# Kernel tuning notes

Measured on AMD Instinct MI355X. Metric: run time of the kernel, lower is better.

Reference implementation:

```python
import jax, jax.numpy as jnp
import numpy as np

N, F, H, K, O = 16384, 64, 128, 16, 10


def setup_inputs() -> dict:
    key = jax.random.key(0)
    ks = jax.random.split(key, 12)
    s = lambda fan: 1.0 / np.sqrt(fan)
    return {
        "x": jax.random.normal(ks[0], (N, F), dtype=jnp.float32),
        "edge_index": jax.random.randint(ks[1], (2, N * 8), 0, N),  # unused by forward
        "mlp_w1": jax.random.normal(ks[2], (2 * F, H), dtype=jnp.float32) * s(2 * F),
        "mlp_b1": jnp.zeros((H,), jnp.float32),
        "mlp_w2": jax.random.normal(ks[3], (H, H), dtype=jnp.float32) * s(H),
        "mlp_b2": jnp.zeros((H,), jnp.float32),
        "gcn_w": jax.random.normal(ks[4], (H, H), dtype=jnp.float32) * s(H),
        "gcn_b": jnp.zeros((H,), jnp.float32),
        "gnn_out_w": jax.random.normal(ks[5], (H, H), dtype=jnp.float32) * s(H),
        "gnn_out_b": jnp.zeros((H,), jnp.float32),
        "out_w": jax.random.normal(ks[6], (H, O), dtype=jnp.float32) * s(H),
        "out_b": jnp.zeros((O,), jnp.float32),
        "k": K,
    }


def _forward(x, mlp_w1, mlp_b1, mlp_w2, mlp_b2, gcn_w, gcn_b,
             gnn_out_w, gnn_out_b, out_w, out_b, k):
    n = x.shape[0]
    # ---- dynamic kNN graph in feature space (includes self, dist 0) ----
    sq = jnp.sum(x * x, axis=-1)                       # [N]
    d2 = sq[:, None] + sq[None, :] - 2.0 * (x @ x.T)   # [N,N] squared dists
    _, idx = jax.lax.top_k(-d2, k)                     # [N,k] neighbor (source) ids per query
    # ---- EdgeConv message: MLP(cat(x_i, x_j - x_i)), max-aggregate over k ----
    x_j = x[idx]                                       # [N,k,F]
    x_i = jnp.broadcast_to(x[:, None, :], x_j.shape)   # [N,k,F]
    m = jnp.concatenate([x_i, x_j - x_i], axis=-1)     # [N,k,2F]
    m = jax.nn.relu(m @ mlp_w1 + mlp_b1)
    m = jax.nn.log_softmax(m @ mlp_w2 + mlp_b2, axis=-1)
    h = jnp.max(m, axis=1)                             # [N,H] max aggregation
    # ---- GCNConv on the kNN edge_index (+ self loops, symmetric norm) ----
    loop = jnp.arange(n)
    src = jnp.concatenate([idx.reshape(-1), loop])     # sources (x_j)
    dst = jnp.concatenate([jnp.repeat(loop, k), loop]) # targets (x_i)
    deg = jax.ops.segment_sum(jnp.ones_like(src, h.dtype), dst, num_segments=n)
    dinv = jax.lax.rsqrt(jnp.maximum(deg, 1.0))
    norm = dinv[src] * dinv[dst]                       # [E]
    hw = h @ gcn_w                                     # [N,H]
    h = jax.ops.segment_sum(norm[:, None] * hw[src], dst, num_segments=n) + gcn_b
    # ---- inner GNN output head (Linear + Softmax) ----
    h = jax.nn.softmax(h @ gnn_out_w + gnn_out_b, axis=-1)
    # ---- GNN_Combo output head (Linear + Softmax) ----
    return jax.nn.softmax(h @ out_w + out_b, axis=-1)  # [N,O]


def reference(x, edge_index, mlp_w1, mlp_b1, mlp_w2, mlp_b2, gcn_w, gcn_b,
              gnn_out_w, gnn_out_b, out_w, out_b, k):
    # edge_index is accepted by GNN_Combo.forward but unused (kNN graph replaces it)
    del edge_index
    return _forward(x, mlp_w1, mlp_b1, mlp_w2, mlp_b2, gcn_w, gcn_b,
                    gnn_out_w, gnn_out_b, out_w, out_b, k)
```

## Files before the change

kernel.cpp:

```cpp
#include <hip/hip_runtime.h>
#include <hip/hip_fp16.h>
#include <cfloat>
#include <cmath>
#include <string.h>


#define N_NODES 16384
#define F_IN    64
#define H_DIM   128
#define K_NN    16
#define O_DIM   10

typedef _Float16 half8  __attribute__((ext_vector_type(8)));
typedef _Float16 half4v __attribute__((ext_vector_type(4)));
typedef _Float16 half2v __attribute__((ext_vector_type(2)));
typedef float    floatx4 __attribute__((ext_vector_type(4)));

__device__ __forceinline__ void async_copy16(void* lds, const void* g) {
  __builtin_amdgcn_global_load_lds(
      (const __attribute__((address_space(1))) unsigned int*)g,
      (__attribute__((address_space(3))) unsigned int*)lds, 16, 0, 0);
}

__device__ __forceinline__ unsigned pack2h(float a, float b) {
  half2v p; p[0] = (_Float16)a; p[1] = (_Float16)b;
  unsigned u; __builtin_memcpy(&u, &p, 4); return u;
}
__device__ __forceinline__ float unpacklo(unsigned u) {
  half2v p; __builtin_memcpy(&p, &u, 4); return (float)p[0];
}
__device__ __forceinline__ float unpackhi(unsigned u) {
  half2v p; __builtin_memcpy(&p, &u, 4); return (float)p[1];
}

__global__ __launch_bounds__(256) void k_prep(const float* __restrict__ x,
                                              float* __restrict__ sq,
                                              double* __restrict__ sq64,
                                              _Float16* __restrict__ xh,
                                              unsigned* __restrict__ cnt) {
  const int i = blockIdx.x * 256 + threadIdx.x;
  if (i >= N_NODES) return;
  const float4* r = (const float4*)(x + i * F_IN);
  float s = 0.f; double sd = 0.0;
#pragma unroll
  for (int q = 0; q < 16; ++q) {
    const float4 v = r[q];
    s += v.x*v.x + v.y*v.y + v.z*v.z + v.w*v.w;
    sd += (double)v.x*v.x + (double)v.y*v.y + (double)v.z*v.z + (double)v.w*v.w;
    half4v hv;
    hv[0] = (_Float16)v.x; hv[1] = (_Float16)v.y;
    hv[2] = (_Float16)v.z; hv[3] = (_Float16)v.w;
    *(half4v*)(xh + (size_t)i * F_IN + 4 * q) = hv;
  }
  sq[i] = s; sq64[i] = sd; cnt[i] = 0;
}

__global__ __launch_bounds__(256) void k_gemm(const _Float16* __restrict__ xh,
                                              const float* __restrict__ sq,
                                              char* __restrict__ subg) {
  __shared__ __align__(16) _Float16 stage[128 * 64];
  __shared__ float sqs[128];
  const int tid = threadIdx.x;
  const int wv = tid >> 6, l = tid & 63;
  const int lane16 = l & 15, quad = l >> 4;
  const int rowblk = (blockIdx.x >> 5) * 256;
  const int seg = blockIdx.x & 31;
  const int rw = rowblk + wv * 64;

  half8 B[4][2];
#pragma unroll
  for (int s = 0; s < 4; ++s) {
    const _Float16* bp = xh + (size_t)(rw + s * 16 + lane16) * F_IN + quad * 8;
    B[s][0] = *(const half8*)(bp);
    B[s][1] = *(const half8*)(bp + 32);
  }

  const int lcol8 = l >> 3;
  const int lchk  = (l & 7) ^ lcol8;
  const size_t lgoff = (size_t)lcol8 * F_IN + lchk * 8;

  for (int tile = 0; tile < 4; ++tile) {
    const int c0 = seg * 512 + tile * 128;
    __syncthreads();
    if (tid < 128) sqs[tid] = sq[c0 + tid];
#pragma unroll
    for (int q = 0; q < 4; ++q) {
      const int grp = wv * 4 + q;
      async_copy16(stage + grp * 512,
                   xh + (size_t)(c0 + grp * 8) * F_IN + lgoff);
    }
    __syncthreads();

    float sprev[4];
    unsigned pk[4][4];
#pragma unroll
    for (int st = 0; st < 8; ++st) {
      const _Float16* base = stage + (st * 16 + lane16) * 64;
      const int sw = lane16 & 7;
      const half8 A0 = *(const half8*)(base + ((quad ^ sw) * 8));
      const half8 A1 = *(const half8*)(base + (((4 + quad) ^ sw) * 8));
      const floatx4 sq4 = *(const floatx4*)(sqs + st * 16 + quad * 4);
      floatx4 acc[4];
#pragma unroll
      for (int s = 0; s < 4; ++s) acc[s] = (floatx4)0.f;
#pragma unroll
      for (int s = 0; s < 4; ++s)
        acc[s] = __builtin_amdgcn_mfma_f32_16x16x32_f16(A0, B[s][0], acc[s], 0, 0, 0);
#pragma unroll
      for (int s = 0; s < 4; ++s)
        acc[s] = __builtin_amdgcn_mfma_f32_16x16x32_f16(A1, B[s][1], acc[s], 0, 0, 0);
#pragma unroll
      for (int s = 0; s < 4; ++s) {
        const float k0 = fmaf(-2.f, acc[s][0], sq4[0]);
        const float k1 = fmaf(-2.f, acc[s][1], sq4[1]);
        const float k2 = fmaf(-2.f, acc[s][2], sq4[2]);
        const float k3 = fmaf(-2.f, acc[s][3], sq4[3]);
        float m = fminf(fminf(k0, k1), fminf(k2, k3));
        m = fminf(m, __shfl_xor(m, 16, 64));
        m = fminf(m, __shfl_xor(m, 32, 64));
        if ((st & 1) == 0) sprev[s] = m;
        else pk[s][st >> 1] = pack2h(sprev[s], m);
      }
    }
    unsigned o0 = pk[0][0], o1 = pk[0][1], o2 = pk[0][2], o3 = pk[0][3];
    if (quad == 1) { o0 = pk[1][0]; o1 = pk[1][1]; o2 = pk[1][2]; o3 = pk[1][3]; }
    if (quad == 2) { o0 = pk[2][0]; o1 = pk[2][1]; o2 = pk[2][2]; o3 = pk[2][3]; }
    if (quad == 3) { o0 = pk[3][0]; o1 = pk[3][1]; o2 = pk[3][2]; o3 = pk[3][3]; }
    const int row = rw + quad * 16 + lane16;
    uint4 ov; ov.x = o0; ov.y = o1; ov.z = o2; ov.w = o3;
    *(uint4*)(subg + ((size_t)row * 1024 + seg * 32 + tile * 8) * 2) = ov;
  }
}

__global__ __launch_bounds__(256) void k_filter(const _Float16* __restrict__ xh,
                                                const float* __restrict__ sq,
                                                const char* __restrict__ subg,
                                                unsigned* __restrict__ cnt,
                                                int* __restrict__ cand) {
  const int l = threadIdx.x & 63;
  const int i = blockIdx.x * 4 + (threadIdx.x >> 6);
  const int part = l & 3, c = l >> 2;

  float xi[16];
  {
    const half8* xp = (const half8*)(xh + (size_t)i * F_IN + part * 16);
    const half8 a = xp[0], b = xp[1];
#pragma unroll
    for (int j = 0; j < 8; ++j) { xi[j] = (float)a[j]; xi[8 + j] = (float)b[j]; }
  }
  float subs[16];
  {
    const uint4 a = *(const uint4*)(subg + ((size_t)i * 1024 + l * 16) * 2);
    const uint4 b = *(const uint4*)(subg + ((size_t)i * 1024 + l * 16) * 2 + 16);
    subs[0] = unpacklo(a.x); subs[1] = unpackhi(a.x);
    subs[2] = unpacklo(a.y); subs[3] = unpackhi(a.y);
    subs[4] = unpacklo(a.z); subs[5] = unpackhi(a.z);
    subs[6] = unpacklo(a.w); subs[7] = unpackhi(a.w);
    subs[8] = unpacklo(b.x); subs[9] = unpackhi(b.x);
    subs[10] = unpacklo(b.y); subs[11] = unpackhi(b.y);
    subs[12] = unpacklo(b.z); subs[13] = unpackhi(b.z);
    subs[14] = unpacklo(b.w); subs[15] = unpackhi(b.w);
  }
  float cmin = subs[0];
#pragma unroll
  for (int t = 1; t < 16; ++t) cmin = fminf(cmin, subs[t]);
  int rank = 0;
#pragma unroll 4
  for (int j = 0; j < 64; ++j) {
    const float vj = __shfl(cmin, j, 64);
    rank += (vj < cmin) || (vj == cmin && j < l);
  }
  const unsigned long long rm = __ballot(rank == 15);
  const int srcl = __ffsll((long long)rm) - 1;
  const float thr = __shfl(cmin, srcl, 64) + 0.25f;

  unsigned selmask = 0;
#pragma unroll
  for (int t = 0; t < 16; ++t) selmask |= (subs[t] <= thr) ? (1u << t) : 0u;

  unsigned long long act;
  while ((act = __ballot(selmask != 0)) != 0ull) {
    const int src = __ffsll((long long)act) - 1;
    unsigned m = __shfl(selmask, src, 64);
    if (l == src) selmask = 0;
    while (m) {
      const int b = __ffs(m) - 1; m &= m - 1;
      const int sid = src * 16 + b;
      const int cg = sid * 16 + c;
      float d = 0.f;
      {
        const half8* gp = (const half8*)(xh + (size_t)cg * F_IN + part * 16);
        const half8 g0 = gp[0], g1 = gp[1];
#pragma unroll
        for (int j = 0; j < 8; ++j) {
          d = fmaf(xi[j], (float)g0[j], d);
          d = fmaf(xi[8 + j], (float)g1[j], d);
        }
      }
      d += __shfl_xor(d, 1, 64);
      d += __shfl_xor(d, 2, 64);
      const float key = fmaf(-2.f, d, sq[cg]);
      const bool pred = (part == 0) && (key <= thr);
      const unsigned long long am = __ballot(pred);
      if (am) {
        const int ldr = __ffsll((long long)am) - 1;
        unsigned base = 0;
        if (l == ldr) base = atomicAdd(&cnt[i], (unsigned)__popcll(am));
        base = __shfl(base, ldr, 64);
        if (pred) {
          const unsigned idx = base + (unsigned)__popcll(am & ((1ull << l) - 1ull));
          if (idx < 128u) cand[(size_t)i * 128 + idx] = cg;
        }
      }
    }
  }
}

__global__ __launch_bounds__(128) void k_rescore(const float* __restrict__ x,
                                                 const double* __restrict__ sq64,
                                                 const int* __restrict__ cand,
                                                 const unsigned* __restrict__ cnt,
                                                 int* __restrict__ knn) {
  __shared__ float  xi[F_IN];
  __shared__ double keys[128];
  __shared__ int    ids[128];
  const int i = blockIdx.x, t = threadIdx.x;
  const unsigned cv = cnt[i];
  const int n = (int)(cv < 128u ? cv : 128u);
  if (t < F_IN) xi[t] = x[i * F_IN + t];
  __syncthreads();
  double key = 1e300; int id = 0x7fffffff;
  if (t < n) {
    id = cand[(size_t)i * 128 + t];
    const float4* xc4 = (const float4*)(x + (size_t)id * F_IN);
    double d0 = 0.0, d1 = 0.0, d2 = 0.0, d3 = 0.0;
#pragma unroll
    for (int q = 0; q < 16; ++q) {
      const float4 v = xc4[q];
      d0 += (double)xi[4*q+0] * (double)v.x;
      d1 += (double)xi[4*q+1] * (double)v.y;
      d2 += (double)xi[4*q+2] * (double)v.z;
      d3 += (double)xi[4*q+3] * (double)v.w;
    }
    key = sq64[id] - 2.0 * ((d0 + d1) + (d2 + d3));
  }
  keys[t] = key; ids[t] = id;
  __syncthreads();
  int rank = 0;
  for (int cix = 0; cix < n; ++cix) {
    const double kc = keys[cix]; const int ic = ids[cix];
    rank += (kc < key) || (kc == key && ic < id);
  }
  if (t < n && rank < K_NN) knn[i * K_NN + rank] = id;
}

__global__ __launch_bounds__(256, 2) void k_lin12(const float* __restrict__ x,
                                                  const float* __restrict__ w1,
                                                  const float* __restrict__ b1,
                                                  _Float16* __restrict__ Ph,
                                                  _Float16* __restrict__ Qh) {
  __shared__ float wl[2 * F_IN][H_DIM];
  for (int s = threadIdx.x; s < 2 * F_IN * H_DIM; s += 256) wl[s >> 7][s & 127] = w1[s];
  __syncthreads();
  const int node = blockIdx.x * 32 + (threadIdx.x & 31);
  const int ob = (threadIdx.x >> 5) * 16;
  float accR[16], accQ[16];
#pragma unroll
  for (int o = 0; o < 16; ++o) { accR[o] = 0.f; accQ[o] = 0.f; }
  const float4* xr = (const float4*)(x + node * F_IN);
#define L1STEP(ff, xs) { \
    const float* wt_ = &wl[(ff)][ob]; \
    const float* wb_ = &wl[(ff) + F_IN][ob]; \
    _Pragma("unroll") \
    for (int o = 0; o < 16; o += 4) { \
      const float4 t4 = *(const float4*)(wt_ + o); \
      const float4 b4 = *(const float4*)(wb_ + o); \
      accR[o+0] = fmaf((xs), t4.x, accR[o+0]); accQ[o+0] = fmaf((xs), b4.x, accQ[o+0]); \
      accR[o+1] = fmaf((xs), t4.y, accR[o+1]); accQ[o+1] = fmaf((xs), b4.y, accQ[o+1]); \
      accR[o+2] = fmaf((xs), t4.z, accR[o+2]); accQ[o+2] = fmaf((xs), b4.z, accQ[o+2]); \
      accR[o+3] = fmaf((xs), t4.w, accR[o+3]); accQ[o+3] = fmaf((xs), b4.w, accQ[o+3]); } }
#pragma unroll 2
  for (int q = 0; q < 16; ++q) {
    const float4 xv = xr[q];
    L1STEP(4*q+0, xv.x); L1STEP(4*q+1, xv.y); L1STEP(4*q+2, xv.z); L1STEP(4*q+3, xv.w);
  }
#undef L1STEP
  _Float16* pp = Ph + (size_t)node * H_DIM + ob;
  _Float16* qp = Qh + (size_t)node * H_DIM + ob;
#pragma unroll
  for (int o = 0; o < 16; o += 4) {
    half4v hp, hq;
#pragma unroll
    for (int u = 0; u < 4; ++u) {
      hp[u] = (_Float16)(accR[o+u] - accQ[o+u] + b1[ob + o + u]);
      hq[u] = (_Float16)accQ[o+u];
    }
    *(half4v*)(pp + o) = hp;
    *(half4v*)(qp + o) = hq;
  }
}

__global__ __launch_bounds__(256, 2) void k_edgeconv(const _Float16* __restrict__ Ph,
                                                     const _Float16* __restrict__ Qh,
                                                     const float* __restrict__ w2,
                                                     const float* __restrict__ b2,
                                                     const int* __restrict__ knn,
                                                     float* __restrict__ h) {
  __shared__ __align__(16) _Float16 wt[H_DIM * 128];
  __shared__ __align__(16) _Float16 afr[4][2048];
  const int tid = threadIdx.x;
  const int wv = tid >> 6, l = tid & 63;
  const int lane16 = l & 15, quad = l >> 4;

  {
    const int n = tid >> 1, part = tid & 1;
    const float* wsrc = w2 + n;
    _Float16* wdst = wt + n * 128;
#pragma unroll
    for (int c = 0; c < 8; ++c) {
      half8 hv;
#pragma unroll
      for (int u = 0; u < 8; ++u)
        hv[u] = (_Float16)wsrc[(size_t)(part * 64 + c * 8 + u) * H_DIM];
      *(half8*)(wdst + (((part * 8 + c) ^ (n & 15)) * 8)) = hv;
    }
  }
  __syncthreads();

  float b2r[8];
#pragma unroll
  for (int tile = 0; tile < 8; ++tile) b2r[tile] = b2[tile * 16 + lane16];

  const int i0 = blockIdx.x * 32 + wv * 8;
  int js[8];
#pragma unroll
  for (int it = 0; it < 8; ++it) js[it] = knn[(i0 + it) * K_NN + lane16];

  _Float16* aw = afr[wv];
  half8 pc[4], qc[4];
  {
    const half8* pr = (const half8*)(Ph + (size_t)i0 * H_DIM + quad * 32);
    const half8* qr = (const half8*)(Qh + (size_t)js[0] * H_DIM + quad * 32);
#pragma unroll
    for (int c = 0; c < 4; ++c) { pc[c] = pr[c]; qc[c] = qr[c]; }
  }
  for (int it = 0; it < 8; ++it) {
    const int i = i0 + it;
    half8 pn[4], qn[4];
    if (it < 7) {
      const half8* pr = (const half8*)(Ph + (size_t)(i + 1) * H_DIM + quad * 32);
      const half8* qr = (const half8*)(Qh + (size_t)js[it + 1] * H_DIM + quad * 32);
#pragma unroll
      for (int c = 0; c < 4; ++c) { pn[c] = pr[c]; qn[c] = qr[c]; }
    }
#pragma unroll
    for (int c = 0; c < 4; ++c) {
      half8 z = pc[c] + qc[c];
      half8 r;
#pragma unroll
      for (int u = 0; u < 8; ++u) r[u] = z[u] > (_Float16)0 ? z[u] : (_Float16)0;
      *(half8*)(aw + quad * 512 + c * 128 + lane16 * 8) = r;
    }
    half8 A[4];
#pragma unroll
    for (int kb = 0; kb < 4; ++kb) A[kb] = *(const half8*)(aw + kb * 512 + l * 8);
    floatx4 acc[8];
#pragma unroll
    for (int tile = 0; tile < 8; ++tile) acc[tile] = (floatx4)0.f;
#pragma unroll
    for (int kb = 0; kb < 4; ++kb) {
#pragma unroll
      for (int tile = 0; tile < 8; ++tile) {
        const half8 B = *(const half8*)(wt + (tile * 16 + lane16) * 128 +
                                        (((kb * 4 + quad) ^ lane16) * 8));
        acc[tile] = __builtin_amdgcn_mfma_f32_16x16x32_f16(A[kb], B, acc[tile], 0, 0, 0);
      }
    }
    float lse[4];
#pragma unroll
    for (int r = 0; r < 4; ++r) {
      float mx = acc[0][r] + b2r[0];
#pragma unroll
      for (int tile = 1; tile < 8; ++tile) mx = fmaxf(mx, acc[tile][r] + b2r[tile]);
      mx = fmaxf(mx, __shfl_xor(mx, 1, 64));
      mx = fmaxf(mx, __shfl_xor(mx, 2, 64));
      mx = fmaxf(mx, __shfl_xor(mx, 4, 64));
      mx = fmaxf(mx, __shfl_xor(mx, 8, 64));
      float e = 0.f;
#pragma unroll
      for (int tile = 0; tile < 8; ++tile) e += __expf(acc[tile][r] + b2r[tile] - mx);
      e += __shfl_xor(e, 1, 64);
      e += __shfl_xor(e, 2, 64);
      e += __shfl_xor(e, 4, 64);
      e += __shfl_xor(e, 8, 64);
      lse[r] = mx + __logf(e);
    }
#pragma unroll
    for (int tile = 0; tile < 8; ++tile) {
      float v = acc[tile][0] + b2r[tile] - lse[0];
#pragma unroll
      for (int r = 1; r < 4; ++r) v = fmaxf(v, acc[tile][r] + b2r[tile] - lse[r]);
      v = fmaxf(v, __shfl_xor(v, 16, 64));
      v = fmaxf(v, __shfl_xor(v, 32, 64));
      if (quad == 0) h[(size_t)i * H_DIM + tile * 16 + lane16] = v;
    }
#pragma unroll
    for (int c = 0; c < 4; ++c) { pc[c] = pn[c]; qc[c] = qn[c]; }
  }
}

__global__ __launch_bounds__(256) void k_hw(const float* __restrict__ h,
                                            const float* __restrict__ gw,
                                            _Float16* __restrict__ hwh) {
  __shared__ float wl[H_DIM][H_DIM];
  for (int s = threadIdx.x; s < H_DIM * H_DIM; s += 256) wl[s >> 7][s & 127] = gw[s];
  __syncthreads();
  const int node = blockIdx.x * 32 + (threadIdx.x & 31);
  const int ob = (threadIdx.x >> 5) * 16;
  float acc[16];
#pragma unroll
  for (int o = 0; o < 16; ++o) acc[o] = 0.f;
  const float4* hr = (const float4*)(h + node * H_DIM);
#define HWSTEP(ff, xs) { \
    const float* wr = &wl[(ff)][ob]; \
    _Pragma("unroll") \
    for (int o = 0; o < 16; o += 4) { const float4 w4 = *(const float4*)(wr + o); \
      acc[o+0] = fmaf((xs), w4.x, acc[o+0]); \
      acc[o+1] = fmaf((xs), w4.y, acc[o+1]); \
      acc[o+2] = fmaf((xs), w4.z, acc[o+2]); \
      acc[o+3] = fmaf((xs), w4.w, acc[o+3]); } }
#pragma unroll 2
  for (int q = 0; q < 32; ++q) {
    const float4 hv = hr[q];
    HWSTEP(4*q+0, hv.x); HWSTEP(4*q+1, hv.y); HWSTEP(4*q+2, hv.z); HWSTEP(4*q+3, hv.w);
  }
#undef HWSTEP
  _Float16* dp = hwh + (size_t)node * H_DIM + ob;
#pragma unroll
  for (int o = 0; o < 16; o += 4) {
    half4v hv;
#pragma unroll
    for (int u = 0; u < 4; ++u) hv[u] = (_Float16)acc[o + u];
    *(half4v*)(dp + o) = hv;
  }
}

__global__ __launch_bounds__(256) void k_heads(const _Float16* __restrict__ hwh,
                                               const int* __restrict__ knn,
                                               const float* __restrict__ gb,
                                               const float* __restrict__ gow,
                                               const float* __restrict__ gob,
                                               const float* __restrict__ ow,
                                               const float* __restrict__ obv,
                                               float* __restrict__ out) {
  __shared__ unsigned int wgo[H_DIM][64];
  __shared__ float hbuf[4][H_DIM];
  for (int s = threadIdx.x; s < H_DIM * 64; s += 256) {
    const int f = s >> 6, l = s & 63;
    wgo[f][l] = pack2h(gow[f * H_DIM + 2 * l], gow[f * H_DIM + 2 * l + 1]);
  }
  __syncthreads();
  const int wv = threadIdx.x >> 6, l = threadIdx.x & 63;
  const unsigned* hw32 = (const unsigned*)hwh;
  const float gbl = gb[2 * l], gbh = gb[2 * l + 1];
  const float gobl = gob[2 * l], gobh = gob[2 * l + 1];
  for (int it = 0; it < 8; ++it) {
    const int i = blockIdx.x * 32 + wv * 8 + it;
    const int* kr = knn + i * K_NN;
    unsigned u = hw32[(size_t)i * 64 + l];
    float s0 = unpacklo(u), s1 = unpackhi(u);
#pragma unroll
    for (int m = 0; m < K_NN; ++m) {
      const unsigned um = hw32[(size_t)kr[m] * 64 + l];
      s0 += unpacklo(um);
      s1 += unpackhi(um);
    }
    const float hg0 = s0 * (1.0f / 17.0f) + gbl;
    const float hg1 = s1 * (1.0f / 17.0f) + gbh;
    hbuf[wv][2 * l] = hg0; hbuf[wv][2 * l + 1] = hg1;
    float z0 = gobl, z1 = gobh;
#pragma unroll 4
    for (int f = 0; f < H_DIM; ++f) {
      const float hv = hbuf[wv][f];
      const unsigned int wvv = wgo[f][l];
      z0 = fmaf(hv, unpacklo(wvv), z0);
      z1 = fmaf(hv, unpackhi(wvv), z1);
    }
    float mx = fmaxf(z0, z1);
#pragma unroll
    for (int s = 1; s < 64; s <<= 1) mx = fmaxf(mx, __shfl_xor(mx, s, 64));
    const float e0 = __expf(z0 - mx), e1 = __expf(z1 - mx);
    float sm = e0 + e1;
#pragma unroll
    for (int s = 1; s < 64; s <<= 1) sm += __shfl_xor(sm, s, 64);
    const float h20 = e0 / sm, h21 = e1 / sm;
    float zc[O_DIM];
#pragma unroll
    for (int c = 0; c < O_DIM; ++c) {
      float a = h20 * ow[(2 * l) * O_DIM + c] + h21 * ow[(2 * l + 1) * O_DIM + c];
#pragma unroll
      for (int s = 1; s < 64; s <<= 1) a += __shfl_xor(a, s, 64);
      zc[c] = a + obv[c];
    }
    float m10 = zc[0];
#pragma unroll
    for (int c = 1; c < O_DIM; ++c) m10 = fmaxf(m10, zc[c]);
    float es[O_DIM]; float s10 = 0.f;
#pragma unroll
    for (int c = 0; c < O_DIM; ++c) { es[c] = __expf(zc[c] - m10); s10 += es[c]; }
    const float inv = 1.0f / s10;
    if (l < O_DIM) {
      float v = es[0];
#pragma unroll
      for (int c = 1; c < O_DIM; ++c) if (l == c) v = es[c];
      out[i * O_DIM + l] = v * inv;
    }
  }
}

extern "C" void kernel_launch(void* const* d_in, const int* in_sizes, int n_in,
                              void* d_out, int out_size, void* d_ws, size_t ws_size,
                              hipStream_t stream) {
  (void)in_sizes; (void)n_in; (void)out_size; (void)ws_size;
  const float* x   = (const float*)d_in[0];
  const float* w1  = (const float*)d_in[2];
  const float* b1  = (const float*)d_in[3];
  const float* w2  = (const float*)d_in[4];
  const float* b2  = (const float*)d_in[5];
  const float* gw  = (const float*)d_in[6];
  const float* gb  = (const float*)d_in[7];
  const float* gow = (const float*)d_in[8];
  const float* gob = (const float*)d_in[9];
  const float* ow  = (const float*)d_in[10];
  const float* obv = (const float*)d_in[11];
  float* out = (float*)d_out;

  char* ws = (char*)d_ws;
  constexpr size_t MB = 1024 * 1024;
  constexpr size_t OFF_SQ   = 0;
  constexpr size_t OFF_SQ64 = OFF_SQ   + (size_t)N_NODES * 4;
  constexpr size_t OFF_XH   = OFF_SQ64 + (size_t)N_NODES * 8;
  constexpr size_t OFF_CNT  = OFF_XH   + (size_t)N_NODES * F_IN * 2;
  constexpr size_t OFF_CAND = OFF_CNT  + (size_t)N_NODES * 4;
  constexpr size_t OFF_SUBG = OFF_CAND + (size_t)N_NODES * 128 * 4;
  constexpr size_t OFF_KNN  = OFF_SUBG;
  constexpr size_t OFF_H    = OFF_SUBG + 1 * MB;
  constexpr size_t OFF_HWH  = OFF_SUBG + 9 * MB;
  float*     sq   = (float*)    (ws + OFF_SQ);
  double*    sq64 = (double*)   (ws + OFF_SQ64);
  _Float16*  xh   = (_Float16*) (ws + OFF_XH);
  unsigned*  cnt  = (unsigned*) (ws + OFF_CNT);
  int*       cand = (int*)      (ws + OFF_CAND);
  char*      subg = (char*)     (ws + OFF_SUBG);
  int*       knn  = (int*)      (ws + OFF_KNN);
  float*     h    = (float*)    (ws + OFF_H);
  _Float16*  hwh  = (_Float16*) (ws + OFF_HWH);
  _Float16*  Ph   = (_Float16*) (ws + OFF_CAND);
  _Float16*  Qh   = (_Float16*) (ws + OFF_CAND + 4 * MB);

  k_prep    <<<N_NODES / 256, 256, 0, stream>>>(x, sq, sq64, xh, cnt);
  k_gemm    <<<2048,          256, 0, stream>>>(xh, sq, subg);
  k_filter  <<<N_NODES / 4,   256, 0, stream>>>(xh, sq, subg, cnt, cand);
  k_rescore <<<N_NODES,       128, 0, stream>>>(x, sq64, cand, cnt, knn);
  k_lin12   <<<N_NODES / 32,  256, 0, stream>>>(x, w1, b1, Ph, Qh);
  k_edgeconv<<<N_NODES / 32,  256, 0, stream>>>(Ph, Qh, w2, b2, knn, h);
  k_hw      <<<N_NODES / 32,  256, 0, stream>>>(h, gw, hwh);
  k_heads   <<<N_NODES / 32,  256, 0, stream>>>(hwh, knn, gb, gow, gob, ow, obv, out);
}
```

Before: 349.4 us.

## Coarsen kNN summary to 32-column groups and restructure filter candidate scan

The distance kernel now reduces minima over 32-column groups instead of 16, halving the summary size. It writes that summary in a segment-major transposed layout through LDS so the global stores are coalesced. The filter kernel reads the smaller summary and builds a per-wave candidate list in shared memory. It then walks the list with software prefetch of the next column tile, using 2 lanes per column and packed fp16 dot2 instructions. The coarser groups mean each selected group covers more columns, so the filter may evaluate more candidates per row in exchange for less summary traffic and fewer reduction shuffles.

New measurement: 355.2 us. Within noise of the previous version (+1.6%).

```diff
diff --git a/kernel.cpp b/kernel.cpp
--- a/kernel.cpp
+++ b/kernel.cpp
@@ -14,6 +14,7 @@
 typedef _Float16 half8  __attribute__((ext_vector_type(8)));
 typedef _Float16 half4v __attribute__((ext_vector_type(4)));
 typedef _Float16 half2v __attribute__((ext_vector_type(2)));
+typedef __fp16   fp16x2 __attribute__((ext_vector_type(2)));
 typedef float    floatx4 __attribute__((ext_vector_type(4)));
 
 __device__ __forceinline__ void async_copy16(void* lds, const void* g) {
@@ -31,6 +32,9 @@
 }
 __device__ __forceinline__ float unpackhi(unsigned u) {
   half2v p; __builtin_memcpy(&p, &u, 4); return (float)p[1];
+}
+__device__ __forceinline__ fp16x2 as_h2(unsigned u) {
+  fp16x2 p; __builtin_memcpy(&p, &u, 4); return p;
 }
 
 __global__ __launch_bounds__(256) void k_prep(const float* __restrict__ x,
@@ -79,6 +83,9 @@
   const int lchk  = (l & 7) ^ lcol8;
   const size_t lgoff = (size_t)lcol8 * F_IN + lchk * 8;
 
+  unsigned sel[8];
+
+#pragma unroll
   for (int tile = 0; tile < 4; ++tile) {
     const int c0 = seg * 512 + tile * 128;
     __syncthreads();
@@ -92,7 +99,8 @@
     __syncthreads();
 
     float sprev[4];
-    unsigned pk[4][4];
+    float sprev2[4];
+    unsigned pk2[4][2];
 #pragma unroll
     for (int st = 0; st < 8; ++st) {
       const _Float16* base = stage + (st * 16 + lane16) * 64;
@@ -115,20 +123,45 @@
         const float k1 = fmaf(-2.f, acc[s][1], sq4[1]);
         const float k2 = fmaf(-2.f, acc[s][2], sq4[2]);
         const float k3 = fmaf(-2.f, acc[s][3], sq4[3]);
-        float m = fminf(fminf(k0, k1), fminf(k2, k3));
-        m = fminf(m, __shfl_xor(m, 16, 64));
-        m = fminf(m, __shfl_xor(m, 32, 64));
-        if ((st & 1) == 0) sprev[s] = m;
-        else pk[s][st >> 1] = pack2h(sprev[s], m);
+        const float m = fminf(fminf(k0, k1), fminf(k2, k3));
+        if ((st & 1) == 0) {
+          sprev[s] = m;
+        } else {
+          float m32 = fminf(sprev[s], m);
+          m32 = fminf(m32, __shfl_xor(m32, 16, 64));
+          m32 = fminf(m32, __shfl_xor(m32, 32, 64));
+          const int g = st >> 1;
+          if ((g & 1) == 0) sprev2[s] = m32;
+          else pk2[s][g >> 1] = pack2h(sprev2[s], m32);
+        }
       }
     }
-    unsigned o0 = pk[0][0], o1 = pk[0][1], o2 = pk[0][2], o3 = pk[0][3];
-    if (quad == 1) { o0 = pk[1][0]; o1 = pk[1][1]; o2 = pk[1][2]; o3 = pk[1][3]; }
-    if (quad == 2) { o0 = pk[2][0]; o1 = pk[2][1]; o2 = pk[2][2]; o3 = pk[2][3]; }
-    if (quad == 3) { o0 = pk[3][0]; o1 = pk[3][1]; o2 = pk[3][2]; o3 = pk[3][3]; }
-    const int row = rw + quad * 16 + lane16;
-    uint4 ov; ov.x = o0; ov.y = o1; ov.z = o2; ov.w = o3;
-    *(uint4*)(subg + ((size_t)row * 1024 + seg * 32 + tile * 8) * 2) = ov;
+#pragma unroll
+    for (int t = 0; t < 2; ++t) {
+      unsigned o = pk2[0][t];
+      if (quad == 1) o = pk2[1][t];
+      if (quad == 2) o = pk2[2][t];
+      if (quad == 3) o = pk2[3][t];
+      sel[tile * 2 + t] = o;
+    }
+  }
+  __syncthreads();
+  {
+    unsigned* sc = (unsigned*)stage + wv * 512;
+#pragma unroll
+    for (int k = 0; k < 8; ++k) sc[k * 64 + l] = sel[k];
+    char* dstw = subg + ((size_t)seg * N_NODES + rw) * 32;
+#pragma unroll
+    for (int t = 0; t < 2; ++t) {
+      const int rl = t * 32 + (l >> 1);
+      const int kb = (l & 1) * 4;
+      uint4 ov;
+      ov.x = sc[(kb + 0) * 64 + rl];
+      ov.y = sc[(kb + 1) * 64 + rl];
+      ov.z = sc[(kb + 2) * 64 + rl];
+      ov.w = sc[(kb + 3) * 64 + rl];
+      *(uint4*)(dstw + t * 1024 + l * 16) = ov;
+    }
   }
 }
 
@@ -137,33 +170,34 @@
                                                 const char* __restrict__ subg,
                                                 unsigned* __restrict__ cnt,
                                                 int* __restrict__ cand) {
+  __shared__ int list[4][128];
+  __shared__ int wcnt[4];
   const int l = threadIdx.x & 63;
-  const int i = blockIdx.x * 4 + (threadIdx.x >> 6);
-  const int part = l & 3, c = l >> 2;
-
-  float xi[16];
+  const int wv = threadIdx.x >> 6;
+  const int i = blockIdx.x * 4 + wv;
+  const int part = l & 1, c = l >> 1;
+
+  fp16x2 xi2[16];
   {
-    const half8* xp = (const half8*)(xh + (size_t)i * F_IN + part * 16);
-    const half8 a = xp[0], b = xp[1];
-#pragma unroll
-    for (int j = 0; j < 8; ++j) { xi[j] = (float)a[j]; xi[8 + j] = (float)b[j]; }
-  }
-  float subs[16];
+    const uint4* xp = (const uint4*)(xh + (size_t)i * F_IN + part * 32);
+#pragma unroll
+    for (int q = 0; q < 4; ++q) {
+      const uint4 a = xp[q];
+      xi2[q*4+0] = as_h2(a.x); xi2[q*4+1] = as_h2(a.y);
+      xi2[q*4+2] = as_h2(a.z); xi2[q*4+3] = as_h2(a.w);
+    }
+  }
+  float subs[8];
   {
-    const uint4 a = *(const uint4*)(subg + ((size_t)i * 1024 + l * 16) * 2);
-    const uint4 b = *(const uint4*)(subg + ((size_t)i * 1024 + l * 16) * 2 + 16);
+    const uint4 a = *(const uint4*)(subg + ((size_t)(l >> 1) * N_NODES + i) * 32 + (l & 1) * 16);
     subs[0] = unpacklo(a.x); subs[1] = unpackhi(a.x);
     subs[2] = unpacklo(a.y); subs[3] = unpackhi(a.y);
     subs[4] = unpacklo(a.z); subs[5] = unpackhi(a.z);
     subs[6] = unpacklo(a.w); subs[7] = unpackhi(a.w);
-    subs[8] = unpacklo(b.x); subs[9] = unpackhi(b.x);
-    subs[10] = unpacklo(b.y); subs[11] = unpackhi(b.y);
-    subs[12] = unpacklo(b.z); subs[13] = unpackhi(b.z);
-    subs[14] = unpacklo(b.w); subs[15] = unpackhi(b.w);
   }
   float cmin = subs[0];
 #pragma unroll
-  for (int t = 1; t < 16; ++t) cmin = fminf(cmin, subs[t]);
+  for (int t = 1; t < 8; ++t) cmin = fminf(cmin, subs[t]);
   int rank = 0;
 #pragma unroll 4
   for (int j = 0; j < 64; ++j) {
@@ -176,44 +210,69 @@
 
   unsigned selmask = 0;
 #pragma unroll
-  for (int t = 0; t < 16; ++t) selmask |= (subs[t] <= thr) ? (1u << t) : 0u;
-
-  unsigned long long act;
-  while ((act = __ballot(selmask != 0)) != 0ull) {
-    const int src = __ffsll((long long)act) - 1;
-    unsigned m = __shfl(selmask, src, 64);
-    if (l == src) selmask = 0;
+  for (int t = 0; t < 8; ++t) selmask |= (subs[t] <= thr) ? (1u << t) : 0u;
+
+  if (l == 0) wcnt[wv] = 0;
+  int base = 0;
+  if (selmask) base = atomicAdd(&wcnt[wv], __popc(selmask));
+  {
+    unsigned m = selmask; int idx = base;
     while (m) {
       const int b = __ffs(m) - 1; m &= m - 1;
-      const int sid = src * 16 + b;
-      const int cg = sid * 16 + c;
-      float d = 0.f;
-      {
-        const half8* gp = (const half8*)(xh + (size_t)cg * F_IN + part * 16);
-        const half8 g0 = gp[0], g1 = gp[1];
-#pragma unroll
-        for (int j = 0; j < 8; ++j) {
-          d = fmaf(xi[j], (float)g0[j], d);
-          d = fmaf(xi[8 + j], (float)g1[j], d);
-        }
+      if (idx < 128) list[wv][idx] = l * 8 + b;
+      ++idx;
+    }
+  }
+  int n = wcnt[wv]; if (n > 128) n = 128;
+
+#define DECODE_COLBASE(e, cb) { \
+    const int src_ = (e) >> 3, b_ = (e) & 7; \
+    const int k_ = (src_ & 1) * 4 + (b_ >> 1); \
+    const int sid_ = (k_ >> 1) * 4 + (k_ & 1) * 2 + (b_ & 1); \
+    cb = (src_ >> 1) * 512 + sid_ * 32; }
+  uint4 g0[4], g1[4];
+  int colc = 0, coln = 0;
+  if (n > 0) {
+    DECODE_COLBASE(list[wv][0], colc);
+    const uint4* gp = (const uint4*)(xh + (size_t)(colc + c) * F_IN + part * 32);
+#pragma unroll
+    for (int q = 0; q < 4; ++q) g0[q] = gp[q];
+  }
+  for (int j = 0; j < n; ++j) {
+    if (j + 1 < n) {
+      DECODE_COLBASE(list[wv][j + 1], coln);
+      const uint4* gp = (const uint4*)(xh + (size_t)(coln + c) * F_IN + part * 32);
+#pragma unroll
+      for (int q = 0; q < 4; ++q) g1[q] = gp[q];
+    }
+    float d = 0.f;
+#pragma unroll
+    for (int q = 0; q < 4; ++q) {
+      d = __builtin_amdgcn_fdot2(xi2[q*4+0], as_h2(g0[q].x), d, false);
+      d = __builtin_amdgcn_fdot2(xi2[q*4+1], as_h2(g0[q].y), d, false);
+      d = __builtin_amdgcn_fdot2(xi2[q*4+2], as_h2(g0[q].z), d, false);
+      d = __builtin_amdgcn_fdot2(xi2[q*4+3], as_h2(g0[q].w), d, false);
+    }
+    d += __shfl_xor(d, 1, 64);
+    const int cg = colc + c;
+    const float key = fmaf(-2.f, d, sq[cg]);
+    const bool pred = (part == 0) && (key <= thr);
+    const unsigned long long am = __ballot(pred);
+    if (am) {
+      const int ldr = __ffsll((long long)am) - 1;
+      unsigned cbase = 0;
+      if (l == ldr) cbase = atomicAdd(&cnt[i], (unsigned)__popcll(am));
+      cbase = __shfl(cbase, ldr, 64);
+      if (pred) {
+        const unsigned idx = cbase + (unsigned)__popcll(am & ((1ull << l) - 1ull));
+        if (idx < 128u) cand[(size_t)i * 128 + idx] = cg;
       }
-      d += __shfl_xor(d, 1, 64);
-      d += __shfl_xor(d, 2, 64);
-      const float key = fmaf(-2.f, d, sq[cg]);
-      const bool pred = (part == 0) && (key <= thr);
-      const unsigned long long am = __ballot(pred);
-      if (am) {
-        const int ldr = __ffsll((long long)am) - 1;
-        unsigned base = 0;
-        if (l == ldr) base = atomicAdd(&cnt[i], (unsigned)__popcll(am));
-        base = __shfl(base, ldr, 64);
-        if (pred) {
-          const unsigned idx = base + (unsigned)__popcll(am & ((1ull << l) - 1ull));
-          if (idx < 128u) cand[(size_t)i * 128 + idx] = cg;
-        }
-      }
-    }
-  }
+    }
+    colc = coln;
+#pragma unroll
+    for (int q = 0; q < 4; ++q) g0[q] = g1[q];
+  }
+#undef DECODE_COLBASE
 }
 
 __global__ __launch_bounds__(128) void k_rescore(const float* __restrict__ x,
```
